# Kernel optimization log

Measured on AMD Instinct MI355X. Metric: run time of the kernel, lower is better.

Reference implementation:

```python
import jax, jax.numpy as jnp
import numpy as np

N_NODES = 50000


def gcn_conv(x, src, dst, W, b, n):
    # PyG GCNConv: h = x @ W; add self-loops; sym-norm aggregate; + bias
    h = x @ W
    loop = jnp.arange(n, dtype=src.dtype)
    s = jnp.concatenate([src, loop])
    d = jnp.concatenate([dst, loop])
    deg = jax.ops.segment_sum(jnp.ones(s.shape[0], h.dtype), d, num_segments=n)
    dinv = jnp.where(deg > 0, jax.lax.rsqrt(deg), 0.0)
    norm = dinv[s] * dinv[d]  # [E+n]
    msg = h[s] * norm[:, None]  # [E+n, C] gather
    out = jax.ops.segment_sum(msg, d, num_segments=n)  # scatter-add
    return out + b


def mlp_decode(z, src, dst, Wa, ba, Wb, bb):
    feat = jnp.concatenate([z[src], z[dst]], axis=1)  # [P, 2*out]
    hid = jax.nn.relu(feat @ Wa + ba)
    return hid @ Wb + bb  # [P, 1]


def setup_inputs() -> dict:
    key = jax.random.key(0)
    ks = jax.random.split(key, 12)
    in_c, hid_c, out_c = 128, 128, 64
    E, P = 800000, 200000
    x = jax.random.normal(ks[0], (N_NODES, in_c), dtype=jnp.float32)
    edge_index = jax.random.randint(ks[1], (2, E), 0, N_NODES, dtype=jnp.int64)
    pos_edge_index = jax.random.randint(ks[2], (2, P), 0, N_NODES, dtype=jnp.int64)
    neg_edge_index = jax.random.randint(ks[3], (2, P), 0, N_NODES, dtype=jnp.int64)
    s1 = 1.0 / np.sqrt(in_c)
    s2 = 1.0 / np.sqrt(hid_c)
    s3 = 1.0 / np.sqrt(2 * out_c)
    W1 = jax.random.uniform(ks[4], (in_c, hid_c), jnp.float32, -s1, s1)
    b1 = jnp.zeros((hid_c,), jnp.float32)
    W2 = jax.random.uniform(ks[5], (hid_c, out_c), jnp.float32, -s2, s2)
    b2 = jnp.zeros((out_c,), jnp.float32)
    Wa = jax.random.uniform(ks[6], (2 * out_c, hid_c), jnp.float32, -s3, s3)
    ba = jax.random.uniform(ks[7], (hid_c,), jnp.float32, -s3, s3)
    Wb = jax.random.uniform(ks[8], (hid_c, 1), jnp.float32, -s2, s2)
    bb = jax.random.uniform(ks[9], (1,), jnp.float32, -s2, s2)
    return {"x": x, "edge_index": edge_index, "pos_edge_index": pos_edge_index,
            "neg_edge_index": neg_edge_index, "W1": W1, "b1": b1, "W2": W2,
            "b2": b2, "Wa": Wa, "ba": ba, "Wb": Wb, "bb": bb}


def reference(x, edge_index, pos_edge_index, neg_edge_index,
              W1, b1, W2, b2, Wa, ba, Wb, bb):
    src, dst = edge_index[0], edge_index[1]
    n = x.shape[0]
    z = gcn_conv(x, src, dst, W1, b1, n)
    z = jax.nn.relu(z)  # dropout disabled in eval mode
    z = gcn_conv(z, src, dst, W2, b2, n)
    pos_pred = mlp_decode(z, pos_edge_index[0], pos_edge_index[1], Wa, ba, Wb, bb)
    neg_pred = mlp_decode(z, neg_edge_index[0], neg_edge_index[1], Wa, ba, Wb, bb)
    return (pos_pred, neg_pred)
```

## Files before the change

kernel.cpp:

```cpp
#include <hip/hip_runtime.h>
#include <hip/hip_bf16.h>
#include <hip/hip_fp16.h>

#define NODES 50000
#define NEDGE 800000
#define NPRED 200000

typedef __attribute__((ext_vector_type(8))) short bf16x8;
typedef __attribute__((ext_vector_type(8))) unsigned short u16x8;
typedef __attribute__((ext_vector_type(4))) float f32x4;

__device__ inline float bf2f(unsigned short u) {
    union { unsigned int i; float f; } v; v.i = ((unsigned int)u) << 16; return v.f;
}
__device__ inline unsigned short f2bf(float f) {
    __hip_bfloat16 b = __float2bfloat16(f);
    return *(unsigned short*)&b;
}
__device__ inline float h2f(unsigned short u) {
    __half h = *(__half*)&u; return __half2float(h);
}
__device__ inline unsigned short f2h(float f) {
    __half h = __float2half(f); return *(unsigned short*)&h;
}

__global__ __launch_bounds__(256) void deg_init(int* __restrict__ deg, int n) {
    int i = blockIdx.x * 256 + threadIdx.x;
    if (i < n) deg[i] = 1;
}

__global__ __launch_bounds__(256) void deg_count4(const int* __restrict__ dstv, int* __restrict__ deg, int E4) {
    int i = blockIdx.x * 256 + threadIdx.x;
    if (i < E4) {
        int4 d4 = ((const int4*)dstv)[i];
        atomicAdd(&deg[d4.x], 1);
        atomicAdd(&deg[d4.y], 1);
        atomicAdd(&deg[d4.z], 1);
        atomicAdd(&deg[d4.w], 1);
    }
}

__global__ __launch_bounds__(256) void scan_bsum(const int* __restrict__ deg, int* __restrict__ bsum, int n) {
    __shared__ int s[256];
    int t = threadIdx.x, b = blockIdx.x;
    int base = b * 1024 + t * 4;
    int sum = 0;
#pragma unroll
    for (int j = 0; j < 4; ++j) { int i = base + j; if (i < n) sum += deg[i] - 1; }
    s[t] = sum; __syncthreads();
    for (int off = 128; off >= 1; off >>= 1) {
        if (t < off) s[t] += s[t + off];
        __syncthreads();
    }
    if (t == 0) bsum[b] = s[0];
}

__global__ void scan_boff(const int* __restrict__ bsum, int* __restrict__ boff, int nb,
                          int* __restrict__ row_ptr, int n) {
    int t = threadIdx.x;
    int v = (t < nb) ? bsum[t] : 0;
    int orig = v;
    for (int off = 1; off < 64; off <<= 1) {
        int u = __shfl_up(v, off, 64);
        if (t >= off) v += u;
    }
    boff[t] = v - orig;
    if (t == 63) row_ptr[n] = v;
}

__global__ __launch_bounds__(256) void scan_write(const int* __restrict__ deg, const int* __restrict__ boff,
                                                  int* __restrict__ row_ptr, int* __restrict__ fillc,
                                                  float* __restrict__ dinv, int n) {
    __shared__ int s[256];
    int t = threadIdx.x, b = blockIdx.x;
    int base = b * 1024 + t * 4;
    int v[4]; int sum = 0;
#pragma unroll
    for (int j = 0; j < 4; ++j) { int i = base + j; v[j] = (i < n) ? (deg[i] - 1) : 0; sum += v[j]; }
    s[t] = sum; __syncthreads();
    for (int off = 1; off < 256; off <<= 1) {
        int u = (t >= off) ? s[t - off] : 0;
        __syncthreads();
        s[t] += u;
        __syncthreads();
    }
    int run = s[t] - sum + boff[b];
#pragma unroll
    for (int j = 0; j < 4; ++j) {
        int i = base + j;
        if (i < n) {
            row_ptr[i] = run; fillc[i] = run; run += v[j];
            dinv[i] = rsqrtf((float)deg[i]);
        }
    }
}

__global__ __launch_bounds__(256) void csr_fill(const int* __restrict__ ei,
                                                int* __restrict__ fillc, int* __restrict__ colv, int E) {
    int e = blockIdx.x * 256 + threadIdx.x;
    if (e < E) {
        int s = ei[e];
        int d = ei[E + e];
        int p = atomicAdd(&fillc[d], 1);
        colv[p] = s;
    }
}

__global__ __launch_bounds__(256) void perm_all(const float* __restrict__ W1, const float* __restrict__ W2,
                                                const float* __restrict__ Wa,
                                                unsigned short* __restrict__ pW1,
                                                unsigned short* __restrict__ pW2,
                                                unsigned short* __restrict__ pWa) {
    int t = blockIdx.x * 256 + threadIdx.x;
    if (t >= 5120) return;
    if (t < 3072) {
        const float* W; unsigned short* P; int N;
        if (t < 2048) { W = W1; P = pW1; N = 128; }
        else          { W = W2; P = pW2; N = 64; t -= 2048; }
        int lane = t & 63;
        int kt = (t >> 6) & 3;
        int nt = t >> 8;
        int n = nt * 16 + (lane & 15);
        int k0 = kt * 32 + (lane >> 4) * 8;
#pragma unroll
        for (int j = 0; j < 8; ++j) P[t * 8 + j] = f2bf(W[(k0 + j) * N + n]);
    } else {
        int tt = t - 3072;
        int h = tt >> 10;
        int r = tt & 1023;
        int lane = r & 63;
        int kt = (r >> 6) & 1;
        int nt = r >> 7;
        int n = nt * 16 + (lane & 15);
        int k0 = h * 64 + kt * 32 + (lane >> 4) * 8;
#pragma unroll
        for (int j = 0; j < 8; ++j) pWa[tt * 8 + j] = f2bf(Wa[(k0 + j) * 128 + n]);
    }
}

template <int NT, bool AFP32>
__global__ __launch_bounds__(256) void gemm_mfma(const void* __restrict__ Xv,
                                                 const unsigned short* __restrict__ perm,
                                                 unsigned short* __restrict__ H, int M) {
    int w = blockIdx.x * 4 + (threadIdx.x >> 6);
    int m0 = w * 16;
    if (m0 >= M) return;
    int lane = threadIdx.x & 63;
    int m = lane & 15, q = lane >> 4;
    size_t row = (size_t)(m0 + m);
    bf16x8 a[4];
    if (AFP32) {
        const float* X = (const float*)Xv;
#pragma unroll
        for (int kt = 0; kt < 4; ++kt) {
            float4 f0 = *(const float4*)&X[row * 128 + kt * 32 + q * 8];
            float4 f1 = *(const float4*)&X[row * 128 + kt * 32 + q * 8 + 4];
            bf16x8 av;
            av[0] = (short)f2bf(f0.x); av[1] = (short)f2bf(f0.y);
            av[2] = (short)f2bf(f0.z); av[3] = (short)f2bf(f0.w);
            av[4] = (short)f2bf(f1.x); av[5] = (short)f2bf(f1.y);
            av[6] = (short)f2bf(f1.z); av[7] = (short)f2bf(f1.w);
            a[kt] = av;
        }
    } else {
        const unsigned short* X = (const unsigned short*)Xv;
#pragma unroll
        for (int kt = 0; kt < 4; ++kt)
            a[kt] = *(const bf16x8*)&X[row * 128 + kt * 32 + q * 8];
    }
    const int N = NT * 16;
#pragma unroll
    for (int nt = 0; nt < NT; ++nt) {
        f32x4 c = {0.f, 0.f, 0.f, 0.f};
#pragma unroll
        for (int kt = 0; kt < 4; ++kt) {
            bf16x8 b = *(const bf16x8*)(perm + (size_t)((nt * 4 + kt) * 64 + lane) * 8);
            c = __builtin_amdgcn_mfma_f32_16x16x32_bf16(a[kt], b, c, 0, 0, 0);
        }
#pragma unroll
        for (int r = 0; r < 4; ++r)
            H[(size_t)(m0 + q * 4 + r) * N + nt * 16 + m] = f2bf(c[r]);
    }
}

template <int C, bool RELU>
__global__ __launch_bounds__(256) void agg_bf16(const unsigned short* __restrict__ h,
                                                const int* __restrict__ row_ptr, const int* __restrict__ colv,
                                                const float* __restrict__ dinv, const float* __restrict__ bias,
                                                unsigned short* __restrict__ out) {
    constexpr int TPN = C / 8;
    constexpr int NPB = 256 / TPN;
    int d = blockIdx.x * NPB + threadIdx.x / TPN;
    if (d >= NODES) return;
    int c8 = (threadIdx.x % TPN) * 8;
    float dv = dinv[d];
    float acc[8];
    u16x8 self = *(const u16x8*)&h[(size_t)d * C + c8];
#pragma unroll
    for (int j = 0; j < 8; ++j) acc[j] = bf2f(self[j]) * dv;
    int i = row_ptr[d], end = row_ptr[d + 1];
    for (; i + 3 < end; i += 4) {
        int s0 = colv[i], s1 = colv[i + 1], s2 = colv[i + 2], s3 = colv[i + 3];
        float w0 = dinv[s0], w1 = dinv[s1], w2 = dinv[s2], w3 = dinv[s3];
        u16x8 r0 = *(const u16x8*)&h[(size_t)s0 * C + c8];
        u16x8 r1 = *(const u16x8*)&h[(size_t)s1 * C + c8];
        u16x8 r2 = *(const u16x8*)&h[(size_t)s2 * C + c8];
        u16x8 r3 = *(const u16x8*)&h[(size_t)s3 * C + c8];
#pragma unroll
        for (int j = 0; j < 8; ++j)
            acc[j] += bf2f(r0[j]) * w0 + bf2f(r1[j]) * w1 + bf2f(r2[j]) * w2 + bf2f(r3[j]) * w3;
    }
    for (; i < end; ++i) {
        int s0 = colv[i];
        float w0 = dinv[s0];
        u16x8 r0 = *(const u16x8*)&h[(size_t)s0 * C + c8];
#pragma unroll
        for (int j = 0; j < 8; ++j) acc[j] += bf2f(r0[j]) * w0;
    }
    u16x8 ov;
#pragma unroll
    for (int j = 0; j < 8; ++j) {
        float o = acc[j] * dv + bias[c8 + j];
        if (RELU) o = fmaxf(o, 0.f);
        ov[j] = f2bf(o);
    }
    *(u16x8*)&out[(size_t)d * C + c8] = ov;
}

__global__ __launch_bounds__(256) void uv_gemm(const unsigned short* __restrict__ zb,
                                               const unsigned short* __restrict__ pWa,
                                               unsigned short* __restrict__ U, unsigned short* __restrict__ V,
                                               int M) {
    int w = blockIdx.x * 4 + (threadIdx.x >> 6);
    int m0 = w * 16;
    if (m0 >= M) return;
    int lane = threadIdx.x & 63;
    int m = lane & 15, q = lane >> 4;
    size_t row = (size_t)(m0 + m);
    bf16x8 a0 = *(const bf16x8*)&zb[row * 64 + q * 8];
    bf16x8 a1 = *(const bf16x8*)&zb[row * 64 + 32 + q * 8];
#pragma unroll
    for (int h = 0; h < 2; ++h) {
        unsigned short* O = h ? V : U;
        const unsigned short* p = pWa + (size_t)h * 1024 * 8;
#pragma unroll
        for (int nt = 0; nt < 8; ++nt) {
            bf16x8 b0 = *(const bf16x8*)(p + (size_t)((nt * 2 + 0) * 64 + lane) * 8);
            bf16x8 b1 = *(const bf16x8*)(p + (size_t)((nt * 2 + 1) * 64 + lane) * 8);
            f32x4 c = {0.f, 0.f, 0.f, 0.f};
            c = __builtin_amdgcn_mfma_f32_16x16x32_bf16(a0, b0, c, 0, 0, 0);
            c = __builtin_amdgcn_mfma_f32_16x16x32_bf16(a1, b1, c, 0, 0, 0);
#pragma unroll
            for (int r = 0; r < 4; ++r)
                O[(size_t)(m0 + q * 4 + r) * 128 + nt * 16 + m] = f2h(c[r]);
        }
    }
}

__global__ __launch_bounds__(256) void edge_decode(const unsigned short* __restrict__ U,
                                                   const unsigned short* __restrict__ V,
                                                   const int* __restrict__ pos, const int* __restrict__ neg,
                                                   const float* __restrict__ ba, const float* __restrict__ Wb,
                                                   const float* __restrict__ bb, float* __restrict__ out, int P) {
    __shared__ float sba[128], sWb[128];
    int tid = threadIdx.x;
    if (tid < 128) sba[tid] = ba[tid];
    else sWb[tid - 128] = Wb[tid - 128];
    __syncthreads();
    int half = (blockIdx.x >= 6250);
    const int* src = half ? neg : pos;
    float* o = out + (half ? P : 0);
    int b = half ? (int)blockIdx.x - 6250 : (int)blockIdx.x;
    int lane = tid & 63;
    int wv = tid >> 6;
    int e = b * 32 + wv * 8 + (lane >> 3);
    int ch0 = (lane & 7) * 16;
    int s = src[e], d = src[P + e];
    u16x8 u0 = *(const u16x8*)&U[(size_t)s * 128 + ch0];
    u16x8 u1 = *(const u16x8*)&U[(size_t)s * 128 + ch0 + 8];
    u16x8 v0 = *(const u16x8*)&V[(size_t)d * 128 + ch0];
    u16x8 v1 = *(const u16x8*)&V[(size_t)d * 128 + ch0 + 8];
    float acc = 0.f;
#pragma unroll
    for (int j = 0; j < 8; ++j) {
        float a = h2f(u0[j]) + h2f(v0[j]) + sba[ch0 + j];
        acc += fmaxf(a, 0.f) * sWb[ch0 + j];
        float c = h2f(u1[j]) + h2f(v1[j]) + sba[ch0 + 8 + j];
        acc += fmaxf(c, 0.f) * sWb[ch0 + 8 + j];
    }
    acc += __shfl_xor(acc, 1, 64);
    acc += __shfl_xor(acc, 2, 64);
    acc += __shfl_xor(acc, 4, 64);
    if ((lane & 7) == 0) o[e] = acc + bb[0];
}

extern "C" void kernel_launch(void* const* d_in, const int* in_sizes, int n_in,
                              void* d_out, int out_size, void* d_ws, size_t ws_size,
                              hipStream_t stream) {
    const int N = NODES, E = NEDGE, P = NPRED;
    const float* x  = (const float*)d_in[0];
    const int*   ei = (const int*)d_in[1];
    const int*  pos = (const int*)d_in[2];
    const int*  neg = (const int*)d_in[3];
    const float* W1 = (const float*)d_in[4];
    const float* b1 = (const float*)d_in[5];
    const float* W2 = (const float*)d_in[6];
    const float* b2 = (const float*)d_in[7];
    const float* Wa = (const float*)d_in[8];
    const float* ba = (const float*)d_in[9];
    const float* Wb = (const float*)d_in[10];
    const float* bb = (const float*)d_in[11];
    float* out = (float*)d_out;

    char* w = (char*)d_ws;
    auto alloc = [&](size_t bytes) { char* p = w; w += (bytes + 255) & ~(size_t)255; return p; };
    int*   deg     = (int*)alloc((size_t)N * 4);
    int*   fillc   = (int*)alloc((size_t)N * 4);
    int*   row_ptr = (int*)alloc((size_t)(N + 1) * 4);
    int*   colv    = (int*)alloc((size_t)E * 4);
    float* dinv    = (float*)alloc((size_t)N * 4);
    int*   bsum    = (int*)alloc(64 * 4);
    int*   boff    = (int*)alloc(64 * 4);
    unsigned short* h1b = (unsigned short*)alloc((size_t)N * 128 * 2);
    unsigned short* z1b = (unsigned short*)alloc((size_t)N * 128 * 2);
    unsigned short* h2b = (unsigned short*)alloc((size_t)N * 64 * 2);
    unsigned short* zb  = (unsigned short*)alloc((size_t)N * 64 * 2);
    unsigned short* Ut  = (unsigned short*)alloc((size_t)N * 128 * 2);
    unsigned short* Vt  = (unsigned short*)alloc((size_t)N * 128 * 2);
    unsigned short* pW1 = (unsigned short*)alloc(2048 * 8 * 2);
    unsigned short* pW2 = (unsigned short*)alloc(1024 * 8 * 2);
    unsigned short* pWa = (unsigned short*)alloc(2048 * 8 * 2);

    const int nb = (N + 1023) / 1024;
    deg_init<<<(N + 255) / 256, 256, 0, stream>>>(deg, N);
    deg_count4<<<(E / 4 + 255) / 256, 256, 0, stream>>>(ei + E, deg, E / 4);
    scan_bsum<<<nb, 256, 0, stream>>>(deg, bsum, N);
    scan_boff<<<1, 64, 0, stream>>>(bsum, boff, nb, row_ptr, N);
    scan_write<<<nb, 256, 0, stream>>>(deg, boff, row_ptr, fillc, dinv, N);
    csr_fill<<<(E + 255) / 256, 256, 0, stream>>>(ei, fillc, colv, E);

    perm_all<<<20, 256, 0, stream>>>(W1, W2, Wa, pW1, pW2, pWa);

    gemm_mfma<8, true><<<782, 256, 0, stream>>>(x, pW1, h1b, N);
    agg_bf16<128, true><<<N / 16, 256, 0, stream>>>(h1b, row_ptr, colv, dinv, b1, z1b);

    gemm_mfma<4, false><<<782, 256, 0, stream>>>(z1b, pW2, h2b, N);
    agg_bf16<64, false><<<(N + 31) / 32, 256, 0, stream>>>(h2b, row_ptr, colv, dinv, b2, zb);

    uv_gemm<<<782, 256, 0, stream>>>(zb, pWa, Ut, Vt, N);
    edge_decode<<<12500, 256, 0, stream>>>(Ut, Vt, pos, neg, ba, Wb, bb, out, P);
}
```

Measured before the change: 289.1 us.

## Record atomic ranks during degree count and batch four edges per group in decode

The degree-count kernel now keeps the return value of each atomicAdd as a per-edge rank. The CSR fill then places each edge at row_ptr[dst] + rank with plain stores, which removes the second pass of atomics. Vectorized int4 loads replace scalar ones, and hipMemsetAsync replaces the deg_init kernel. The edge decoder now has each 8-lane group handle four edges, keeps bias and weight values in registers instead of LDS, and writes results as float4. The cost is an extra E-sized rank buffer and more registers per thread in the decoder.

```diff
diff --git a/kernel.cpp b/kernel.cpp
--- a/kernel.cpp
+++ b/kernel.cpp
@@ -24,29 +24,27 @@
     __half h = __float2half(f); return *(unsigned short*)&h;
 }
 
-__global__ __launch_bounds__(256) void deg_init(int* __restrict__ deg, int n) {
-    int i = blockIdx.x * 256 + threadIdx.x;
-    if (i < n) deg[i] = 1;
-}
-
-__global__ __launch_bounds__(256) void deg_count4(const int* __restrict__ dstv, int* __restrict__ deg, int E4) {
+__global__ __launch_bounds__(256) void rank_count4(const int* __restrict__ dstv, int* __restrict__ cnt,
+                                                   int* __restrict__ rank, int E4) {
     int i = blockIdx.x * 256 + threadIdx.x;
     if (i < E4) {
         int4 d4 = ((const int4*)dstv)[i];
-        atomicAdd(&deg[d4.x], 1);
-        atomicAdd(&deg[d4.y], 1);
-        atomicAdd(&deg[d4.z], 1);
-        atomicAdd(&deg[d4.w], 1);
-    }
-}
-
-__global__ __launch_bounds__(256) void scan_bsum(const int* __restrict__ deg, int* __restrict__ bsum, int n) {
+        int4 r4;
+        r4.x = atomicAdd(&cnt[d4.x], 1);
+        r4.y = atomicAdd(&cnt[d4.y], 1);
+        r4.z = atomicAdd(&cnt[d4.z], 1);
+        r4.w = atomicAdd(&cnt[d4.w], 1);
+        ((int4*)rank)[i] = r4;
+    }
+}
+
+__global__ __launch_bounds__(256) void scan_bsum(const int* __restrict__ cnt, int* __restrict__ bsum, int n) {
     __shared__ int s[256];
     int t = threadIdx.x, b = blockIdx.x;
     int base = b * 1024 + t * 4;
     int sum = 0;
 #pragma unroll
-    for (int j = 0; j < 4; ++j) { int i = base + j; if (i < n) sum += deg[i] - 1; }
+    for (int j = 0; j < 4; ++j) { int i = base + j; if (i < n) sum += cnt[i]; }
     s[t] = sum; __syncthreads();
     for (int off = 128; off >= 1; off >>= 1) {
         if (t < off) s[t] += s[t + off];
@@ -68,15 +66,14 @@
     if (t == 63) row_ptr[n] = v;
 }
 
-__global__ __launch_bounds__(256) void scan_write(const int* __restrict__ deg, const int* __restrict__ boff,
-                                                  int* __restrict__ row_ptr, int* __restrict__ fillc,
-                                                  float* __restrict__ dinv, int n) {
+__global__ __launch_bounds__(256) void scan_write(const int* __restrict__ cnt, const int* __restrict__ boff,
+                                                  int* __restrict__ row_ptr, float* __restrict__ dinv, int n) {
     __shared__ int s[256];
     int t = threadIdx.x, b = blockIdx.x;
     int base = b * 1024 + t * 4;
     int v[4]; int sum = 0;
 #pragma unroll
-    for (int j = 0; j < 4; ++j) { int i = base + j; v[j] = (i < n) ? (deg[i] - 1) : 0; sum += v[j]; }
+    for (int j = 0; j < 4; ++j) { int i = base + j; v[j] = (i < n) ? cnt[i] : 0; sum += v[j]; }
     s[t] = sum; __syncthreads();
     for (int off = 1; off < 256; off <<= 1) {
         int u = (t >= off) ? s[t - off] : 0;
@@ -89,20 +86,23 @@
     for (int j = 0; j < 4; ++j) {
         int i = base + j;
         if (i < n) {
-            row_ptr[i] = run; fillc[i] = run; run += v[j];
-            dinv[i] = rsqrtf((float)deg[i]);
-        }
-    }
-}
-
-__global__ __launch_bounds__(256) void csr_fill(const int* __restrict__ ei,
-                                                int* __restrict__ fillc, int* __restrict__ colv, int E) {
-    int e = blockIdx.x * 256 + threadIdx.x;
-    if (e < E) {
-        int s = ei[e];
-        int d = ei[E + e];
-        int p = atomicAdd(&fillc[d], 1);
-        colv[p] = s;
+            row_ptr[i] = run; run += v[j];
+            dinv[i] = rsqrtf((float)(v[j] + 1));
+        }
+    }
+}
+
+__global__ __launch_bounds__(256) void csr_fill2(const int* __restrict__ ei, const int* __restrict__ rank,
+                                                 const int* __restrict__ row_ptr, int* __restrict__ colv, int E4) {
+    int i = blockIdx.x * 256 + threadIdx.x;
+    if (i < E4) {
+        int4 s4 = ((const int4*)ei)[i];
+        int4 d4 = ((const int4*)(ei + NEDGE))[i];
+        int4 r4 = ((const int4*)rank)[i];
+        colv[row_ptr[d4.x] + r4.x] = s4.x;
+        colv[row_ptr[d4.y] + r4.y] = s4.y;
+        colv[row_ptr[d4.z] + r4.z] = s4.z;
+        colv[row_ptr[d4.w] + r4.w] = s4.w;
     }
 }
 
@@ -257,41 +257,61 @@
     }
 }
 
-__global__ __launch_bounds__(256) void edge_decode(const unsigned short* __restrict__ U,
-                                                   const unsigned short* __restrict__ V,
-                                                   const int* __restrict__ pos, const int* __restrict__ neg,
-                                                   const float* __restrict__ ba, const float* __restrict__ Wb,
-                                                   const float* __restrict__ bb, float* __restrict__ out, int P) {
-    __shared__ float sba[128], sWb[128];
+__global__ __launch_bounds__(256) void edge_decode2(const unsigned short* __restrict__ U,
+                                                    const unsigned short* __restrict__ V,
+                                                    const int* __restrict__ pos, const int* __restrict__ neg,
+                                                    const float* __restrict__ ba, const float* __restrict__ Wb,
+                                                    const float* __restrict__ bb, float* __restrict__ out, int P) {
     int tid = threadIdx.x;
-    if (tid < 128) sba[tid] = ba[tid];
-    else sWb[tid - 128] = Wb[tid - 128];
-    __syncthreads();
-    int half = (blockIdx.x >= 6250);
+    int grp = tid >> 3;
+    int ch0 = (tid & 7) * 16;
+    float bav[16], wbv[16];
+    *(float4*)&bav[0]  = *(const float4*)&ba[ch0];
+    *(float4*)&bav[4]  = *(const float4*)&ba[ch0 + 4];
+    *(float4*)&bav[8]  = *(const float4*)&ba[ch0 + 8];
+    *(float4*)&bav[12] = *(const float4*)&ba[ch0 + 12];
+    *(float4*)&wbv[0]  = *(const float4*)&Wb[ch0];
+    *(float4*)&wbv[4]  = *(const float4*)&Wb[ch0 + 4];
+    *(float4*)&wbv[8]  = *(const float4*)&Wb[ch0 + 8];
+    *(float4*)&wbv[12] = *(const float4*)&Wb[ch0 + 12];
+    int e0 = blockIdx.x * 128 + grp * 4;
+    int half = (e0 >= P);
     const int* src = half ? neg : pos;
-    float* o = out + (half ? P : 0);
-    int b = half ? (int)blockIdx.x - 6250 : (int)blockIdx.x;
-    int lane = tid & 63;
-    int wv = tid >> 6;
-    int e = b * 32 + wv * 8 + (lane >> 3);
-    int ch0 = (lane & 7) * 16;
-    int s = src[e], d = src[P + e];
-    u16x8 u0 = *(const u16x8*)&U[(size_t)s * 128 + ch0];
-    u16x8 u1 = *(const u16x8*)&U[(size_t)s * 128 + ch0 + 8];
-    u16x8 v0 = *(const u16x8*)&V[(size_t)d * 128 + ch0];
-    u16x8 v1 = *(const u16x8*)&V[(size_t)d * 128 + ch0 + 8];
-    float acc = 0.f;
-#pragma unroll
-    for (int j = 0; j < 8; ++j) {
-        float a = h2f(u0[j]) + h2f(v0[j]) + sba[ch0 + j];
-        acc += fmaxf(a, 0.f) * sWb[ch0 + j];
-        float c = h2f(u1[j]) + h2f(v1[j]) + sba[ch0 + 8 + j];
-        acc += fmaxf(c, 0.f) * sWb[ch0 + 8 + j];
-    }
-    acc += __shfl_xor(acc, 1, 64);
-    acc += __shfl_xor(acc, 2, 64);
-    acc += __shfl_xor(acc, 4, 64);
-    if ((lane & 7) == 0) o[e] = acc + bb[0];
+    int le0 = half ? e0 - P : e0;
+    int s[4], d[4];
+#pragma unroll
+    for (int j = 0; j < 4; ++j) { s[j] = src[le0 + j]; d[j] = src[P + le0 + j]; }
+    u16x8 u0[4], u1[4], v0[4], v1[4];
+#pragma unroll
+    for (int j = 0; j < 4; ++j) {
+        u0[j] = *(const u16x8*)&U[(size_t)s[j] * 128 + ch0];
+        u1[j] = *(const u16x8*)&U[(size_t)s[j] * 128 + ch0 + 8];
+        v0[j] = *(const u16x8*)&V[(size_t)d[j] * 128 + ch0];
+        v1[j] = *(const u16x8*)&V[(size_t)d[j] * 128 + ch0 + 8];
+    }
+    float acc[4];
+#pragma unroll
+    for (int j = 0; j < 4; ++j) {
+        float a = 0.f;
+#pragma unroll
+        for (int k = 0; k < 8; ++k) {
+            float h0 = h2f((unsigned short)u0[j][k]) + h2f((unsigned short)v0[j][k]) + bav[k];
+            a += fmaxf(h0, 0.f) * wbv[k];
+            float h1 = h2f((unsigned short)u1[j][k]) + h2f((unsigned short)v1[j][k]) + bav[8 + k];
+            a += fmaxf(h1, 0.f) * wbv[8 + k];
+        }
+        acc[j] = a;
+    }
+#pragma unroll
+    for (int off = 1; off <= 4; off <<= 1) {
+#pragma unroll
+        for (int j = 0; j < 4; ++j) acc[j] += __shfl_xor(acc[j], off, 64);
+    }
+    if ((tid & 7) == 0) {
+        float bbv = bb[0];
+        float4 st = { acc[0] + bbv, acc[1] + bbv, acc[2] + bbv, acc[3] + bbv };
+        *(float4*)&out[e0] = st;
+    }
 }
 
 extern "C" void kernel_launch(void* const* d_in, const int* in_sizes, int n_in,
@@ -314,8 +334,8 @@
 
     char* w = (char*)d_ws;
     auto alloc = [&](size_t bytes) { char* p = w; w += (bytes + 255) & ~(size_t)255; return p; };
-    int*   deg     = (int*)alloc((size_t)N * 4);
-    int*   fillc   = (int*)alloc((size_t)N * 4);
+    int*   cnt     = (int*)alloc((size_t)N * 4);
+    int*   rankb   = (int*)alloc((size_t)E * 4);
     int*   row_ptr = (int*)alloc((size_t)(N + 1) * 4);
     int*   colv    = (int*)alloc((size_t)E * 4);
     float* dinv    = (float*)alloc((size_t)N * 4);
@@ -332,12 +352,12 @@
     unsigned short* pWa = (unsigned short*)alloc(2048 * 8 * 2);
 
     const int nb = (N + 1023) / 1024;
-    deg_init<<<(N + 255) / 256, 256, 0, stream>>>(deg, N);
-    deg_count4<<<(E / 4 + 255) / 256, 256, 0, stream>>>(ei + E, deg, E / 4);
-    scan_bsum<<<nb, 256, 0, stream>>>(deg, bsum, N);
+    hipMemsetAsync(cnt, 0, (size_t)N * 4, stream);
+    rank_count4<<<(E / 4 + 255) / 256, 256, 0, stream>>>(ei + E, cnt, rankb, E / 4);
+    scan_bsum<<<nb, 256, 0, stream>>>(cnt, bsum, N);
     scan_boff<<<1, 64, 0, stream>>>(bsum, boff, nb, row_ptr, N);
-    scan_write<<<nb, 256, 0, stream>>>(deg, boff, row_ptr, fillc, dinv, N);
-    csr_fill<<<(E + 255) / 256, 256, 0, stream>>>(ei, fillc, colv, E);
+    scan_write<<<nb, 256, 0, stream>>>(cnt, boff, row_ptr, dinv, N);
+    csr_fill2<<<(E / 4 + 255) / 256, 256, 0, stream>>>(ei, rankb, row_ptr, colv, E / 4);
 
     perm_all<<<20, 256, 0, stream>>>(W1, W2, Wa, pW1, pW2, pWa);
 
@@ -348,5 +368,5 @@
     agg_bf16<64, false><<<(N + 31) / 32, 256, 0, stream>>>(h2b, row_ptr, colv, dinv, b2, zb);
 
     uv_gemm<<<782, 256, 0, stream>>>(zb, pWa, Ut, Vt, N);
-    edge_decode<<<12500, 256, 0, stream>>>(Ut, Vt, pos, neg, ba, Wb, bb, out, P);
-}
+    edge_decode2<<<(2 * P) / 128, 256, 0, stream>>>(Ut, Vt, pos, neg, ba, Wb, bb, out, P);
+}
```

New measurement: 252.7 us. 1.14x faster.
